# Kernel tuning notes

Measured on AMD Instinct MI355X. Metric: run time of the kernel, lower is better.

## Reference

```python
import jax, jax.numpy as jnp
import numpy as np

N_NODES = 51200
N_EDGES = 819200
N_GRAPHS = 256


def _p(k, shape, scale=0.05):
    return jax.random.normal(k, shape, jnp.float32) * scale


def setup_inputs() -> dict:
    key = jax.random.key(0)
    ks = jax.random.split(key, 32)
    inp = {
        "x": jax.random.normal(ks[0], (N_NODES, 128), jnp.float32),
        "src": jax.random.randint(ks[1], (N_EDGES,), 0, N_NODES, jnp.int32),
        "dst": jax.random.randint(ks[2], (N_EDGES,), 0, N_NODES, jnp.int32),
        "graph_ids": jnp.sort(jax.random.randint(ks[3], (N_NODES,), 0, N_GRAPHS, jnp.int32)),
        "edge_weight": jax.random.uniform(ks[4], (N_EDGES,), jnp.float32),
        "conv1_w": _p(ks[5], (96, 128, 3)), "conv1_b": _p(ks[6], (96,)),
        "conv2_w": _p(ks[7], (96, 128, 3)), "conv2_b": _p(ks[8], (96,)),
        "conv3_w": _p(ks[9], (96, 128, 3)), "conv3_b": _p(ks[10], (96,)),
        "W11": _p(ks[11], (96, 54)), "b11": _p(ks[12], (54,)),
        "W12": _p(ks[13], (96, 54)), "b12": _p(ks[14], (54,)),
        "W13": _p(ks[15], (96, 54)), "b13": _p(ks[16], (54,)),
        "W2": _p(ks[17], (54, 25)), "b2": _p(ks[18], (25,)),
        "W3": _p(ks[19], (25, 13)), "b3": _p(ks[20], (13,)),
        "W4": _p(ks[21], (25, 11)), "b4": _p(ks[22], (11,)),
        "Wc1": _p(ks[23], (49, 27)), "bc1": _p(ks[24], (27,)),
        "Wc2": _p(ks[25], (27, 5)), "bc2": _p(ks[26], (5,)),
    }
    return inp


def _conv1d(x_ncw, k_oiw, b, dilation, pad):
    # x: [1,128,N], k: [96,128,3] -> [1,96,N]
    y = jax.lax.conv_general_dilated(
        x_ncw, k_oiw, window_strides=(1,), padding=[(pad, pad)],
        rhs_dilation=(dilation,), dimension_numbers=("NCH", "OIH", "NCH"))
    return y + b[None, :, None]


def reference(x, src, dst, graph_ids, edge_weight,
              conv1_w, conv1_b, conv2_w, conv2_b, conv3_w, conv3_b,
              W11, b11, W12, b12, W13, b13, W2, b2, W3, b3, W4, b4,
              Wc1, bc1, Wc2, bc2):
    relu = jax.nn.relu
    h0 = x.T[None]  # [1,128,N] — conv over the batched node sequence, as in torch
    c1 = _conv1d(h0, conv1_w, conv1_b, 1, 1)[0].T  # [N,96]
    c2 = _conv1d(h0, conv2_w, conv2_b, 2, 2)[0].T
    c3 = _conv1d(h0, conv3_w, conv3_b, 3, 3)[0].T
    h01 = relu(c1) + c2
    h02 = relu(c2) + c3
    h03 = relu(c3) + c1

    def gconv(h, W, b):
        # DGL GraphConv norm='none', in>out: transform first, then weighted scatter-sum
        hw = h @ W                              # [N,out]
        msg = hw[src] * edge_weight[:, None]    # [E,out]
        return jax.ops.segment_sum(msg, dst, num_segments=N_NODES) + b

    ac_h1 = relu(gconv(h01, W11, b11)) + relu(gconv(h02, W12, b12)) + relu(gconv(h03, W13, b13))
    ac_h2 = relu(gconv(ac_h1, W2, b2))
    ac_h3 = relu(gconv(ac_h2, W3, b3))
    ac_h4 = relu(gconv(ac_h2, W4, b4))

    seg = lambda v: jax.ops.segment_sum(v, graph_ids, num_segments=N_GRAPHS)
    hg = jnp.concatenate([seg(ac_h2), seg(ac_h3), seg(ac_h4)], axis=1)  # [G,49]
    return (hg @ Wc1 + bc1) @ Wc2 + bc2  # [G,5]
```

## Files before the change

kernel.cpp:

```cpp
#include <hip/hip_runtime.h>
#include <hip/hip_bf16.h>

#define N_NODES 51200
#define N_EDGES 819200
#define N_GRAPHS 256

typedef __attribute__((ext_vector_type(8))) short short8;
typedef __attribute__((ext_vector_type(4))) float f32x4;

__device__ __forceinline__ ushort f2bf(float f) {
    uint u = __builtin_bit_cast(uint, f);
    u += 0x7FFFu + ((u >> 16) & 1u);
    return (ushort)(u >> 16);
}
__device__ __forceinline__ float bf2f(ushort h) {
    uint u = ((uint)h) << 16;
    return __builtin_bit_cast(float, u);
}

__global__ __launch_bounds__(256) void k_init(
    const float* __restrict__ w1, const float* __restrict__ w2,
    const float* __restrict__ w3,
    const float* __restrict__ W11, const float* __restrict__ W12,
    const float* __restrict__ W13,
    const float* __restrict__ b11, const float* __restrict__ b12,
    const float* __restrict__ b13,
    ushort* __restrict__ Wtc, ushort* __restrict__ Wp1,
    float* __restrict__ bias_cat,
    float* __restrict__ hg, int* __restrict__ cnt) {
    int idx = blockIdx.x * 256 + threadIdx.x;
    if (idx < N_GRAPHS * 49) hg[idx] = 0.f;
    if (idx < N_NODES) cnt[idx] = 0;
    if (idx < 176)
        bias_cat[idx] = (idx < 54) ? b11[idx] : (idx < 108) ? b12[idx - 54]
                      : (idx < 162) ? b13[idx - 108] : 0.f;
    if (idx < 3 * 12 * 96 * 32) {
        int kl = idx & 31;
        int o  = (idx >> 5) % 96;
        int s  = (idx >> 5) / 96 % 12;
        int k  = idx / (32 * 96 * 12);
        int kk = s * 32 + kl;
        int t = kk >> 7, i = kk & 127;
        const float* w = (k == 0) ? w1 : (k == 1) ? w2 : w3;
        Wtc[idx] = f2bf(w[(o * 128 + i) * 3 + t]);
    }
    if (idx < 3 * 3 * 64 * 32) {
        int kl = idx & 31;
        int o  = (idx >> 5) % 64;
        int s2 = (idx >> 5) / 64 % 3;
        int k  = idx / (32 * 64 * 3);
        int kk2 = s2 * 32 + kl;
        const float* W = (k == 0) ? W11 : (k == 1) ? W12 : W13;
        Wp1[idx] = (o < 54) ? f2bf(W[kk2 * 54 + o]) : (ushort)0;
    }
}

#define RNG 6400
#define ECHUNK 4096
#define NBLK_CSR (8 * (N_EDGES / ECHUNK))
#define DEG_MAX 64

__global__ __launch_bounds__(256) void k_scatter(
    const int* __restrict__ src, const int* __restrict__ dst,
    const float* __restrict__ ew,
    int* __restrict__ cnt, uint* __restrict__ s_pack) {
    int r = blockIdx.x & 7, c = blockIdx.x >> 3;
    int lo = r * RNG, hi = lo + RNG;
    int base = c * ECHUNK + threadIdx.x;
#pragma unroll
    for (int i = 0; i < ECHUNK / 256; ++i) {
        int e = base + i * 256;
        int d = dst[e];
        int sv = src[e];
        float wv = ew[e];
        if (d >= lo && d < hi) {
            int pos = atomicAdd(&cnt[d], 1);
            if (pos < DEG_MAX)
                s_pack[(d << 6) + pos] = ((uint)f2bf(wv) << 16) | (uint)sv;
        }
    }
}

#define BN 64
#define XS_LD 136
#define HS_LD 104

__global__ __launch_bounds__(256, 4) void k_conv(
    const float* __restrict__ x,
    const ushort* __restrict__ Wtc, const ushort* __restrict__ Wp1g,
    const float* __restrict__ b1, const float* __restrict__ b2,
    const float* __restrict__ b3,
    ushort* __restrict__ hw_cat) {
    __shared__ ushort xs[70 * XS_LD];
    __shared__ ushort wl[9216];
    ushort* wp   = wl;
    ushort* hswb = xs;

    const int tid = threadIdx.x;
    const int n0  = blockIdx.x * BN;

    for (int idx = tid; idx < 70 * 32; idx += 256) {
        int row = idx >> 5, c4 = (idx & 31) << 2;
        int node = n0 - 3 + row;
        float4 v = make_float4(0.f, 0.f, 0.f, 0.f);
        if (node >= 0 && node < N_NODES)
            v = *reinterpret_cast<const float4*>(x + (size_t)node * 128 + c4);
        ushort* p = &xs[row * XS_LD + c4];
        p[0] = f2bf(v.x); p[1] = f2bf(v.y); p[2] = f2bf(v.z); p[3] = f2bf(v.w);
    }

    const int lane = tid & 63;
    const int wave = tid >> 6;
    const int r16  = lane & 15;
    const int b8   = (lane >> 4) * 8;

    f32x4 acc[3][6];
#pragma unroll
    for (int k = 0; k < 3; ++k)
#pragma unroll
        for (int ot = 0; ot < 6; ++ot) acc[k][ot] = (f32x4)0.f;

    ushort4 wreg[9];
#pragma unroll
    for (int i = 0; i < 9; ++i)
        wreg[i] = *reinterpret_cast<const ushort4*>(Wtc + (i * 256 + tid) * 4);

#pragma unroll
    for (int kq = 0; kq < 12; ++kq) {
        const int k = kq >> 2;
        const int q = kq & 3;
        __syncthreads();
#pragma unroll
        for (int i = 0; i < 9; ++i)
            *reinterpret_cast<ushort4*>(wl + (i * 256 + tid) * 4) = wreg[i];
        __syncthreads();
        if (kq < 11) {
            const ushort* nw = Wtc + (size_t)(kq + 1) * 9216;
#pragma unroll
            for (int i = 0; i < 9; ++i)
                wreg[i] = *reinterpret_cast<const ushort4*>(nw + (i * 256 + tid) * 4);
        }
        const int dk = k + 1;
#pragma unroll
        for (int sp = 0; sp < 3; ++sp) {
            const int s     = q * 3 + sp;
            const int cbase = (s * 32) & 127;
            const int t     = (s * 32) >> 7;
            const int roff  = (t - 1) * dk + 3;
            short8 a = *reinterpret_cast<const short8*>(
                &xs[(wave * 16 + r16 + roff) * XS_LD + cbase + b8]);
#pragma unroll
            for (int ot = 0; ot < 6; ++ot) {
                short8 b = *reinterpret_cast<const short8*>(
                    &wl[(sp * 96 + ot * 16 + r16) * 32 + b8]);
                acc[k][ot] = __builtin_amdgcn_mfma_f32_16x16x32_bf16(a, b, acc[k][ot], 0, 0, 0);
            }
        }
    }

#pragma unroll
    for (int ot = 0; ot < 6; ++ot) {
        int o = ot * 16 + r16;
        float bb1 = b1[o], bb2 = b2[o], bb3 = b3[o];
#pragma unroll
        for (int r = 0; r < 4; ++r) {
            float C1 = acc[0][ot][r] + bb1;
            float C2 = acc[1][ot][r] + bb2;
            float C3 = acc[2][ot][r] + bb3;
            acc[0][ot][r] = fmaxf(C1, 0.f) + C2;
            acc[1][ot][r] = fmaxf(C2, 0.f) + C3;
            acc[2][ot][r] = fmaxf(C3, 0.f) + C1;
        }
    }

    ushort* hs = hswb + wave * (16 * HS_LD);
#pragma unroll
    for (int k = 0; k < 3; ++k) {
        __syncthreads();
#pragma unroll
        for (int i = 0; i < 6; ++i)
            *reinterpret_cast<ushort4*>(wp + (i * 256 + tid) * 4) =
                *reinterpret_cast<const ushort4*>(Wp1g + k * 6144 + (i * 256 + tid) * 4);
#pragma unroll
        for (int ot = 0; ot < 6; ++ot)
#pragma unroll
            for (int r = 0; r < 4; ++r)
                hs[((lane >> 4) * 4 + r) * HS_LD + ot * 16 + r16] = f2bf(acc[k][ot][r]);
        __syncthreads();
        f32x4 acc2[4];
#pragma unroll
        for (int ot2 = 0; ot2 < 4; ++ot2) acc2[ot2] = (f32x4)0.f;
#pragma unroll
        for (int s2 = 0; s2 < 3; ++s2) {
            short8 a = *reinterpret_cast<const short8*>(&hs[r16 * HS_LD + s2 * 32 + b8]);
#pragma unroll
            for (int ot2 = 0; ot2 < 4; ++ot2) {
                short8 b = *reinterpret_cast<const short8*>(
                    &wp[(s2 * 64 + ot2 * 16 + r16) * 32 + b8]);
                acc2[ot2] = __builtin_amdgcn_mfma_f32_16x16x32_bf16(a, b, acc2[ot2], 0, 0, 0);
            }
        }
#pragma unroll
        for (int ot2 = 0; ot2 < 4; ++ot2) {
            int co = ot2 * 16 + r16;
            if (co < 54) {
#pragma unroll
                for (int r = 0; r < 4; ++r) {
                    int node = n0 + wave * 16 + (lane >> 4) * 4 + r;
                    hw_cat[(size_t)node * 176 + k * 54 + co] = f2bf(acc2[ot2][r]);
                }
            }
        }
    }
    for (int idx = tid; idx < 64 * 14; idx += 256) {
        int r = idx / 14, c = 162 + (idx - r * 14);
        hw_cat[(size_t)(n0 + r) * 176 + c] = 0;
    }
}

__global__ __launch_bounds__(256) void k_agg1(
    const ushort* __restrict__ hw, const int* __restrict__ cnt,
    const uint* __restrict__ pk, const float* __restrict__ bias_cat,
    const float* __restrict__ W2, ushort* __restrict__ hw2) {
    __shared__ float stage[4][176];
    __shared__ float w2s[54 * 25];
    int tid = threadIdx.x;
    for (int i = tid; i < 54 * 25; i += 256) w2s[i] = W2[i];
    int lane = tid & 63, wave = tid >> 6;
    int n = blockIdx.x * 4 + wave;
    const bool act = lane < 44;
    const int col = lane * 4;
    int e0 = n << 6;
    int e1 = e0 + __builtin_amdgcn_readfirstlane(cnt[n]);
    float a0 = 0.f, a1 = 0.f, a2 = 0.f, a3 = 0.f;
    int e = e0;
    for (; e + 7 < e1; e += 8) {
        uint m[8];
#pragma unroll
        for (int u = 0; u < 8; ++u) m[u] = pk[e + u];
        if (act) {
#pragma unroll
            for (int u = 0; u < 8; ++u) {
                float w = bf2f((ushort)(m[u] >> 16));
                ushort4 v = *reinterpret_cast<const ushort4*>(
                    hw + (size_t)(m[u] & 0xFFFFu) * 176 + col);
                a0 += w * bf2f(v.x); a1 += w * bf2f(v.y);
                a2 += w * bf2f(v.z); a3 += w * bf2f(v.w);
            }
        }
    }
    if (e + 3 < e1) {
        uint m[4];
#pragma unroll
        for (int u = 0; u < 4; ++u) m[u] = pk[e + u];
        if (act) {
#pragma unroll
            for (int u = 0; u < 4; ++u) {
                float w = bf2f((ushort)(m[u] >> 16));
                ushort4 v = *reinterpret_cast<const ushort4*>(
                    hw + (size_t)(m[u] & 0xFFFFu) * 176 + col);
                a0 += w * bf2f(v.x); a1 += w * bf2f(v.y);
                a2 += w * bf2f(v.z); a3 += w * bf2f(v.w);
            }
        }
        e += 4;
    }
    for (; e < e1; ++e) {
        uint m = pk[e];
        if (act) {
            float w = bf2f((ushort)(m >> 16));
            ushort4 v = *reinterpret_cast<const ushort4*>(
                hw + (size_t)(m & 0xFFFFu) * 176 + col);
            a0 += w * bf2f(v.x); a1 += w * bf2f(v.y);
            a2 += w * bf2f(v.z); a3 += w * bf2f(v.w);
        }
    }
    if (act) {
        stage[wave][col + 0] = fmaxf(a0 + bias_cat[col + 0], 0.f);
        stage[wave][col + 1] = fmaxf(a1 + bias_cat[col + 1], 0.f);
        stage[wave][col + 2] = fmaxf(a2 + bias_cat[col + 2], 0.f);
        stage[wave][col + 3] = fmaxf(a3 + bias_cat[col + 3], 0.f);
    }
    __syncthreads();
    if (lane < 54)
        stage[wave][lane] = stage[wave][lane] + stage[wave][lane + 54] +
                            stage[wave][lane + 108];
    if (lane < 25) {
        float acc = 0.f;
#pragma unroll
        for (int i = 0; i < 54; ++i) acc += stage[wave][i] * w2s[i * 25 + lane];
        hw2[(size_t)n * 28 + lane] = f2bf(acc);
    }
}

__global__ __launch_bounds__(256) void k_agg2(
    const ushort* __restrict__ hw2, const int* __restrict__ cnt,
    const uint* __restrict__ pk,
    const float* __restrict__ b2, const float* __restrict__ W3,
    const float* __restrict__ W4, const int* __restrict__ gids,
    ushort* __restrict__ hw34, float* __restrict__ hg) {
    __shared__ float w34s[25 * 24];
    __shared__ float vst[8][26];
    __shared__ int sgid[8];
    int tid = threadIdx.x;
    for (int i = tid; i < 25 * 24; i += 256) {
        int ii = i / 24, j = i - ii * 24;
        w34s[i] = (j < 13) ? W3[ii * 13 + j] : W4[ii * 11 + (j - 13)];
    }
    int lane = tid & 63, wave = tid >> 6;
    int half = lane >> 5, jj = lane & 31;
    int n0b = blockIdx.x * 8;
    int nl = wave * 2 + half;
    int n = n0b + nl;
    int e0 = n << 6;
    int e1 = e0 + cnt[n];
    float acc = 0.f;
    int e = e0;
    for (; e + 7 < e1; e += 8) {
        uint m[8];
#pragma unroll
        for (int u = 0; u < 8; ++u) m[u] = pk[e + u];
        if (jj < 25) {
#pragma unroll
            for (int u = 0; u < 8; ++u)
                acc += bf2f((ushort)(m[u] >> 16)) *
                       bf2f(hw2[(size_t)(m[u] & 0xFFFFu) * 28 + jj]);
        }
    }
    if (e + 3 < e1) {
        uint m[4];
#pragma unroll
        for (int u = 0; u < 4; ++u) m[u] = pk[e + u];
        if (jj < 25) {
#pragma unroll
            for (int u = 0; u < 4; ++u)
                acc += bf2f((ushort)(m[u] >> 16)) *
                       bf2f(hw2[(size_t)(m[u] & 0xFFFFu) * 28 + jj]);
        }
        e += 4;
    }
    for (; e < e1; ++e) {
        uint m = pk[e];
        if (jj < 25) acc += bf2f((ushort)(m >> 16)) *
                            bf2f(hw2[(size_t)(m & 0xFFFFu) * 28 + jj]);
    }
    if (jj < 25) vst[nl][jj] = fmaxf(acc + b2[jj], 0.f);
    if (jj == 0) sgid[nl] = gids[n];
    __syncthreads();
    if (tid < 25) {
        float run = vst[0][tid];
        int g = sgid[0];
        for (int nn = 1; nn < 8; ++nn) {
            if (sgid[nn] == g) run += vst[nn][tid];
            else { atomicAdd(&hg[g * 49 + tid], run); run = vst[nn][tid]; g = sgid[nn]; }
        }
        atomicAdd(&hg[g * 49 + tid], run);
    }
    if (tid < 192) {
        int node = tid / 24, j = tid - node * 24;
        float a = 0.f;
#pragma unroll
        for (int i = 0; i < 25; ++i) a += vst[node][i] * w34s[i * 24 + j];
        hw34[(size_t)(n0b + node) * 24 + j] = f2bf(a);
    }
}

__global__ __launch_bounds__(256) void k_agg34(
    const ushort* __restrict__ hw34, const int* __restrict__ cnt,
    const uint* __restrict__ pk,
    const float* __restrict__ b3, const float* __restrict__ b4,
    const int* __restrict__ gids, float* __restrict__ hg) {
    __shared__ float vst[8][25];
    __shared__ int sgid[8];
    int tid = threadIdx.x;
    int lane = tid & 63, wave = tid >> 6;
    int half = lane >> 5, jj = lane & 31;
    int nl = wave * 2 + half;
    int n = blockIdx.x * 8 + nl;
    int e0 = n << 6;
    int e1 = e0 + cnt[n];
    float acc = 0.f;
    int e = e0;
    for (; e + 7 < e1; e += 8) {
        uint m[8];
#pragma unroll
        for (int u = 0; u < 8; ++u) m[u] = pk[e + u];
        if (jj < 24) {
#pragma unroll
            for (int u = 0; u < 8; ++u)
                acc += bf2f((ushort)(m[u] >> 16)) *
                       bf2f(hw34[(size_t)(m[u] & 0xFFFFu) * 24 + jj]);
        }
    }
    if (e + 3 < e1) {
        uint m[4];
#pragma unroll
        for (int u = 0; u < 4; ++u) m[u] = pk[e + u];
        if (jj < 24) {
#pragma unroll
            for (int u = 0; u < 4; ++u)
                acc += bf2f((ushort)(m[u] >> 16)) *
                       bf2f(hw34[(size_t)(m[u] & 0xFFFFu) * 24 + jj]);
        }
        e += 4;
    }
    for (; e < e1; ++e) {
        uint m = pk[e];
        if (jj < 24) acc += bf2f((ushort)(m >> 16)) *
                            bf2f(hw34[(size_t)(m & 0xFFFFu) * 24 + jj]);
    }
    if (jj < 24) {
        float v = (jj < 13) ? fmaxf(acc + b3[jj], 0.f)
                            : fmaxf(acc + b4[jj - 13], 0.f);
        vst[nl][jj] = v;
    }
    if (jj == 0) sgid[nl] = gids[n];
    __syncthreads();
    if (tid < 24) {
        float run = vst[0][tid];
        int g = sgid[0];
        for (int nn = 1; nn < 8; ++nn) {
            if (sgid[nn] == g) run += vst[nn][tid];
            else { atomicAdd(&hg[g * 49 + 25 + tid], run); run = vst[nn][tid]; g = sgid[nn]; }
        }
        atomicAdd(&hg[g * 49 + 25 + tid], run);
    }
}

__global__ __launch_bounds__(256) void k_final(
    const float* __restrict__ hg, const float* __restrict__ Wc1,
    const float* __restrict__ bc1, const float* __restrict__ Wc2,
    const float* __restrict__ bc2, float* __restrict__ out) {
    int g = blockIdx.x * blockDim.x + threadIdx.x;
    if (g < N_GRAPHS) {
        float t[27];
#pragma unroll
        for (int j = 0; j < 27; ++j) t[j] = bc1[j];
        for (int i = 0; i < 49; ++i) {
            float hv = hg[g * 49 + i];
#pragma unroll
            for (int j = 0; j < 27; ++j) t[j] += hv * Wc1[i * 27 + j];
        }
#pragma unroll
        for (int j2 = 0; j2 < 5; ++j2) {
            float o = bc2[j2];
#pragma unroll
            for (int i = 0; i < 27; ++i) o += t[i] * Wc2[i * 5 + j2];
            out[g * 5 + j2] = o;
        }
    }
}

extern "C" void kernel_launch(void* const* d_in, const int* in_sizes, int n_in,
                              void* d_out, int out_size, void* d_ws, size_t ws_size,
                              hipStream_t stream) {
    const float* x    = (const float*)d_in[0];
    const int*   src  = (const int*)d_in[1];
    const int*   dst  = (const int*)d_in[2];
    const int*   gids = (const int*)d_in[3];
    const float* ew   = (const float*)d_in[4];
    const float* w1 = (const float*)d_in[5],  *b1 = (const float*)d_in[6];
    const float* w2 = (const float*)d_in[7],  *b2 = (const float*)d_in[8];
    const float* w3 = (const float*)d_in[9],  *b3 = (const float*)d_in[10];
    const float* W11 = (const float*)d_in[11], *b11 = (const float*)d_in[12];
    const float* W12 = (const float*)d_in[13], *b12 = (const float*)d_in[14];
    const float* W13 = (const float*)d_in[15], *b13 = (const float*)d_in[16];
    const float* W2  = (const float*)d_in[17], *b2g = (const float*)d_in[18];
    const float* W3  = (const float*)d_in[19], *b3g = (const float*)d_in[20];
    const float* W4  = (const float*)d_in[21], *b4g = (const float*)d_in[22];
    const float* Wc1 = (const float*)d_in[23], *bc1 = (const float*)d_in[24];
    const float* Wc2 = (const float*)d_in[25], *bc2 = (const float*)d_in[26];
    float* out = (float*)d_out;

    char* ws = (char*)d_ws;
    size_t off = 0;
    auto alloc = [&](size_t bytes) {
        size_t o = off;
        off = (off + bytes + 255) & ~(size_t)255;
        return (void*)(ws + o);
    };
    int*    cnt      = (int*)alloc(N_NODES * 4);
    uint*   s_pack   = (uint*)alloc((size_t)N_NODES * DEG_MAX * 4);
    ushort* hw_cat   = (ushort*)alloc((size_t)N_NODES * 176 * 2);
    ushort* hw2      = (ushort*)alloc((size_t)N_NODES * 28 * 2);
    ushort* hw34     = (ushort*)alloc((size_t)N_NODES * 24 * 2);
    float*  hg       = (float*)alloc(N_GRAPHS * 49 * 4);
    ushort* Wtc      = (ushort*)alloc(3 * 12 * 96 * 32 * 2);
    ushort* Wp1      = (ushort*)alloc(3 * 3 * 64 * 32 * 2);
    float*  bias_cat = (float*)alloc(176 * 4);

    k_init<<<(3 * 12 * 96 * 32 + 255) / 256, 256, 0, stream>>>(
        w1, w2, w3, W11, W12, W13, b11, b12, b13, Wtc, Wp1, bias_cat, hg, cnt);
    k_scatter<<<NBLK_CSR, 256, 0, stream>>>(src, dst, ew, cnt, s_pack);
    k_conv<<<N_NODES / BN, 256, 0, stream>>>(x, Wtc, Wp1, b1, b2, b3, hw_cat);
    k_agg1<<<N_NODES / 4, 256, 0, stream>>>(hw_cat, cnt, s_pack,
                                            bias_cat, W2, hw2);
    k_agg2<<<N_NODES / 8, 256, 0, stream>>>(hw2, cnt, s_pack, b2g,
                                            W3, W4, gids, hw34, hg);
    k_agg34<<<N_NODES / 8, 256, 0, stream>>>(hw34, cnt, s_pack, b3g, b4g,
                                             gids, hg);
    k_final<<<1, 256, 0, stream>>>(hg, Wc1, bc1, Wc2, bc2, out);
}
```

Baseline: 202.8 us.

## Fuse edge scatter into conv kernel and prefetch packed edges in agg1

Merges the CSR-building scatter kernel and the conv kernel into one launch. Block groups are interleaved so that two of every three groups of eight blocks do edge scatter and the third computes conv tiles, letting the memory- and atomic-bound scatter overlap with the conv compute. Separately, agg1's edge loop now prefetches the next 8 packed edge entries while the current 8 are processed, hiding index-load latency. The cost is a larger fused kernel whose scatter blocks also reserve the conv's shared memory, which can limit occupancy, plus extra registers held for the prefetch.

```diff
diff --git a/kernel.cpp b/kernel.cpp
--- a/kernel.cpp
+++ b/kernel.cpp
@@ -57,47 +57,49 @@
 
 #define RNG 6400
 #define ECHUNK 4096
-#define NBLK_CSR (8 * (N_EDGES / ECHUNK))
 #define DEG_MAX 64
-
-__global__ __launch_bounds__(256) void k_scatter(
+#define BN 64
+#define XS_LD 136
+#define HS_LD 104
+
+__global__ __launch_bounds__(256, 4) void k_convscat(
+    const float* __restrict__ x,
+    const ushort* __restrict__ Wtc, const ushort* __restrict__ Wp1g,
+    const float* __restrict__ b1, const float* __restrict__ b2,
+    const float* __restrict__ b3, ushort* __restrict__ hw_cat,
     const int* __restrict__ src, const int* __restrict__ dst,
     const float* __restrict__ ew,
     int* __restrict__ cnt, uint* __restrict__ s_pack) {
-    int r = blockIdx.x & 7, c = blockIdx.x >> 3;
-    int lo = r * RNG, hi = lo + RNG;
-    int base = c * ECHUNK + threadIdx.x;
-#pragma unroll
-    for (int i = 0; i < ECHUNK / 256; ++i) {
-        int e = base + i * 256;
-        int d = dst[e];
-        int sv = src[e];
-        float wv = ew[e];
-        if (d >= lo && d < hi) {
-            int pos = atomicAdd(&cnt[d], 1);
-            if (pos < DEG_MAX)
-                s_pack[(d << 6) + pos] = ((uint)f2bf(wv) << 16) | (uint)sv;
-        }
-    }
-}
-
-#define BN 64
-#define XS_LD 136
-#define HS_LD 104
-
-__global__ __launch_bounds__(256, 4) void k_conv(
-    const float* __restrict__ x,
-    const ushort* __restrict__ Wtc, const ushort* __restrict__ Wp1g,
-    const float* __restrict__ b1, const float* __restrict__ b2,
-    const float* __restrict__ b3,
-    ushort* __restrict__ hw_cat) {
     __shared__ ushort xs[70 * XS_LD];
     __shared__ ushort wl[9216];
+
+    const int tid = threadIdx.x;
+    const int gid = blockIdx.x >> 3;
+    const int sub = blockIdx.x & 7;
+
+    if (gid % 3 != 2) {
+        int c = (gid / 3) * 2 + (gid % 3);
+        int lo = sub * RNG, hi = lo + RNG;
+        int base = c * ECHUNK + tid;
+#pragma unroll
+        for (int i = 0; i < ECHUNK / 256; ++i) {
+            int e = base + i * 256;
+            int d = dst[e];
+            int sv = src[e];
+            float wv = ew[e];
+            if (d >= lo && d < hi) {
+                int pos = atomicAdd(&cnt[d], 1);
+                if (pos < DEG_MAX)
+                    s_pack[(d << 6) + pos] = ((uint)f2bf(wv) << 16) | (uint)sv;
+            }
+        }
+        return;
+    }
+
+    const int tile = (gid / 3) * 8 + sub;
+    const int n0   = tile * BN;
     ushort* wp   = wl;
     ushort* hswb = xs;
-
-    const int tid = threadIdx.x;
-    const int n0  = blockIdx.x * BN;
 
     for (int idx = tid; idx < 70 * 32; idx += 256) {
         int row = idx >> 5, c4 = (idx & 31) << 2;
@@ -234,19 +236,31 @@
     int e1 = e0 + __builtin_amdgcn_readfirstlane(cnt[n]);
     float a0 = 0.f, a1 = 0.f, a2 = 0.f, a3 = 0.f;
     int e = e0;
-    for (; e + 7 < e1; e += 8) {
+    if (e + 7 < e1) {
         uint m[8];
 #pragma unroll
         for (int u = 0; u < 8; ++u) m[u] = pk[e + u];
-        if (act) {
-#pragma unroll
-            for (int u = 0; u < 8; ++u) {
-                float w = bf2f((ushort)(m[u] >> 16));
-                ushort4 v = *reinterpret_cast<const ushort4*>(
-                    hw + (size_t)(m[u] & 0xFFFFu) * 176 + col);
-                a0 += w * bf2f(v.x); a1 += w * bf2f(v.y);
-                a2 += w * bf2f(v.z); a3 += w * bf2f(v.w);
-            }
+        for (;;) {
+            bool more = (e + 15 < e1);
+            uint mn[8];
+            if (more) {
+#pragma unroll
+                for (int u = 0; u < 8; ++u) mn[u] = pk[e + 8 + u];
+            }
+            if (act) {
+#pragma unroll
+                for (int u = 0; u < 8; ++u) {
+                    float w = bf2f((ushort)(m[u] >> 16));
+                    ushort4 v = *reinterpret_cast<const ushort4*>(
+                        hw + (size_t)(m[u] & 0xFFFFu) * 176 + col);
+                    a0 += w * bf2f(v.x); a1 += w * bf2f(v.y);
+                    a2 += w * bf2f(v.z); a3 += w * bf2f(v.w);
+                }
+            }
+            e += 8;
+            if (!more) break;
+#pragma unroll
+            for (int u = 0; u < 8; ++u) m[u] = mn[u];
         }
     }
     if (e + 3 < e1) {
@@ -491,8 +505,8 @@
 
     k_init<<<(3 * 12 * 96 * 32 + 255) / 256, 256, 0, stream>>>(
         w1, w2, w3, W11, W12, W13, b11, b12, b13, Wtc, Wp1, bias_cat, hg, cnt);
-    k_scatter<<<NBLK_CSR, 256, 0, stream>>>(src, dst, ew, cnt, s_pack);
-    k_conv<<<N_NODES / BN, 256, 0, stream>>>(x, Wtc, Wp1, b1, b2, b3, hw_cat);
+    k_convscat<<<2400, 256, 0, stream>>>(x, Wtc, Wp1, b1, b2, b3, hw_cat,
+                                         src, dst, ew, cnt, s_pack);
     k_agg1<<<N_NODES / 4, 256, 0, stream>>>(hw_cat, cnt, s_pack,
                                             bias_cat, W2, hw2);
     k_agg2<<<N_NODES / 8, 256, 0, stream>>>(hw2, cnt, s_pack, b2g,
```

Measured after the change: 195.3 us, median of 2. -3.7%, faster.
